# Kernel optimization log

Hardware: AMD Instinct MI355X
Metric: run time of the kernel (lower is better)

Reference implementation:

```python
import jax, jax.numpy as jnp
import numpy as np

BN_EPS = 1e-3      # Keras BatchNormalization default epsilon
LRELU_ALPHA = 0.3  # Keras LeakyReLU default alpha


def _bn(x, gamma, beta, mean, var):
    # inference-mode batch norm over the feature (last) axis
    return gamma * (x - mean) * jax.lax.rsqrt(var + BN_EPS) + beta


def _gcn(x, adj, w, b):
    # spektral GCNConv: A_hat @ (X @ W) + b   (adj assumed pre-normalized)
    xw = jnp.einsum('bnf,fc->bnc', x, w)
    return jnp.einsum('bnm,bmc->bnc', adj, xw) + b


def _lrelu(x):
    return jnp.where(x >= 0, x, LRELU_ALPHA * x)


def setup_inputs() -> dict:
    key = jax.random.key(0)
    ks = jax.random.split(key, 12)
    B, N, C = 16, 1024, 256
    x = jax.random.normal(ks[0], (B, N, C), dtype=jnp.float32)
    # roughly row-normalized dense adjacency (stands in for D^-1/2 (A+I) D^-1/2)
    adj = jax.random.uniform(ks[1], (B, N, N), dtype=jnp.float32) / N
    s = 1.0 / np.sqrt(C)
    return {
        'x': x,
        'adj': adj,
        'bn1_gamma': jnp.ones((C,), jnp.float32),
        'bn1_beta': jnp.zeros((C,), jnp.float32),
        'bn1_mean': jax.random.normal(ks[2], (C,), jnp.float32) * 0.1,
        'bn1_var': jax.random.uniform(ks[3], (C,), jnp.float32) + 0.5,
        'w1': jax.random.normal(ks[4], (C, C), jnp.float32) * s,
        'b1': jnp.zeros((C,), jnp.float32),
        'bn2_gamma': jnp.ones((C,), jnp.float32),
        'bn2_beta': jnp.zeros((C,), jnp.float32),
        'bn2_mean': jax.random.normal(ks[5], (C,), jnp.float32) * 0.1,
        'bn2_var': jax.random.uniform(ks[6], (C,), jnp.float32) + 0.5,
        'w2': jax.random.normal(ks[7], (C, C), jnp.float32) * s,
        'b2': jnp.zeros((C,), jnp.float32),
        'w_skip': jax.random.normal(ks[8], (C, C), jnp.float32) * s,
        'b_skip': jnp.zeros((C,), jnp.float32),
    }


def reference(x, adj, bn1_gamma, bn1_beta, bn1_mean, bn1_var, w1, b1,
              bn2_gamma, bn2_beta, bn2_mean, bn2_var, w2, b2, w_skip, b_skip):
    h = _bn(x, bn1_gamma, bn1_beta, bn1_mean, bn1_var)          # BN(input)
    out = _lrelu(_gcn(h, adj, w1, b1))                          # GCNConv + LeakyReLU
    out = _bn(out, bn2_gamma, bn2_beta, bn2_mean, bn2_var)      # BN
    out = _lrelu(_gcn(out, adj, w2, b2))                        # GCNConv + LeakyReLU
    skip = _gcn(h, adj, w_skip, b_skip)                         # skip GCNConv on BN(input)
    # Dropout is identity at inference
    return out + skip
```

## Files before the change

### kernel.cpp

```cpp
#include <hip/hip_runtime.h>

#define LRELU_ALPHA 0.3f
#define BN_EPS 1e-3f

using u16 = unsigned short;
using u32 = unsigned int;

typedef __attribute__((ext_vector_type(8))) short bf16x8;
typedef __attribute__((ext_vector_type(4))) float f32x4;

struct alignas(8) U16x4 { u16 x, y, z, w; };

__device__ __forceinline__ u16 f2bf(float f) {
  union { float f; u32 u; } v; v.f = f;
  u32 b = v.u;
  b += 0x7FFFu + ((b >> 16) & 1u);
  return (u16)(b >> 16);
}
__device__ __forceinline__ float bf2f(u16 h) {
  union { u32 u; float f; } v; v.u = ((u32)h) << 16;
  return v.f;
}

typedef const __attribute__((address_space(1))) void* gas_ptr;
typedef __attribute__((address_space(3))) void* las_ptr;

__device__ __forceinline__ void gload16(const void* g, void* l) {
  __builtin_amdgcn_global_load_lds((gas_ptr)g, (las_ptr)l, 16, 0, 0);
}

template <int K>
__device__ __forceinline__ void gemm_core(const u16* __restrict__ A,
                                          const u16* __restrict__ B,
                                          u16* lds,
                                          f32x4 (&acc)[4][4]) {
  const int t    = threadIdx.x;
  const int lane = t & 63;
  const int wid  = t >> 6;
  const int wm   = (wid >> 1) * 64;
  const int wn   = (wid & 1) * 64;
  const int lrow = lane & 15;
  const int lk   = (lane >> 4) * 8;

  const int r0 = t >> 3;
  const int ce = (t & 7) * 8;
  const int lo = (t >> 6) * 512;

  auto stage = [&](int buf, int kt) {
    u16* ldsA = lds + buf * 16384;
    u16* ldsB = ldsA + 8192;
    const u16* gA = A + kt * 64;
    const u16* gB = B + kt * 64;
#pragma unroll
    for (int cc = 0; cc < 4; ++cc) {
      gload16(gA + (size_t)(cc * 32 + r0) * K + ce, ldsA + cc * 2048 + lo);
      gload16(gB + (size_t)(cc * 32 + r0) * K + ce, ldsB + cc * 2048 + lo);
    }
  };

  auto compute = [&](int buf) {
    const u16* As = lds + buf * 16384;
    const u16* Bs = As + 8192;
#pragma unroll
    for (int kk = 0; kk < 2; ++kk) {
      bf16x8 a[4], b[4];
#pragma unroll
      for (int i = 0; i < 4; ++i)
        a[i] = *(const bf16x8*)(As + (wm + i * 16 + lrow) * 64 + kk * 32 + lk);
#pragma unroll
      for (int i = 0; i < 4; ++i)
        b[i] = *(const bf16x8*)(Bs + (wn + i * 16 + lrow) * 64 + kk * 32 + lk);
#pragma unroll
      for (int i = 0; i < 4; ++i)
#pragma unroll
        for (int j = 0; j < 4; ++j)
          acc[i][j] = __builtin_amdgcn_mfma_f32_16x16x32_bf16(a[i], b[j], acc[i][j], 0, 0, 0);
    }
  };

  const int KT = K / 64;
  stage(0, 0);
  asm volatile("s_waitcnt vmcnt(0)" ::: "memory");
  __syncthreads();
  int cur = 0;
#pragma unroll 1
  for (int kt = 0; kt < KT - 1; ++kt) {
    stage(cur ^ 1, kt + 1);
    compute(cur);
    asm volatile("s_waitcnt vmcnt(0)" ::: "memory");
    __syncthreads();
    cur ^= 1;
  }
  compute(cur);
}

#define ACC_INIT()                                  \
  f32x4 acc[4][4];                                  \
  _Pragma("unroll") for (int i_ = 0; i_ < 4; ++i_)  \
  _Pragma("unroll") for (int j_ = 0; j_ < 4; ++j_)  \
      acc[i_][j_] = {0.f, 0.f, 0.f, 0.f};

__global__ void k_prep_bn(const float* __restrict__ g1, const float* __restrict__ be1,
                          const float* __restrict__ m1, const float* __restrict__ v1,
                          const float* __restrict__ g2, const float* __restrict__ be2,
                          const float* __restrict__ m2, const float* __restrict__ v2,
                          float* __restrict__ s1, float* __restrict__ t1,
                          float* __restrict__ s2, float* __restrict__ t2c) {
  int c = threadIdx.x;
  float a1 = g1[c] * rsqrtf(v1[c] + BN_EPS);
  s1[c] = a1; t1[c] = be1[c] - m1[c] * a1;
  float a2 = g2[c] * rsqrtf(v2[c] + BN_EPS);
  s2[c] = a2; t2c[c] = be2[c] - m2[c] * a2;
}

__global__ void k_prep_w(const float* __restrict__ w1, const float* __restrict__ wsk,
                         const float* __restrict__ w2,
                         u16* __restrict__ wcatT, u16* __restrict__ w2T) {
  int i = blockIdx.x * 256 + threadIdx.x;
  if (i < 131072) {
    int co = i >> 8, ci = i & 255;
    const float* w = (co < 256) ? w1 : wsk;
    wcatT[i] = f2bf(w[ci * 256 + (co & 255)]);
  } else if (i < 196608) {
    int k = i - 131072;
    int co = k >> 8, ci = k & 255;
    w2T[k] = f2bf(w2[ci * 256 + co]);
  }
}

__global__ void k_convert(const float* __restrict__ adj, const float* __restrict__ x,
                          const float* __restrict__ s1, const float* __restrict__ t1,
                          u16* __restrict__ adj_bf, u16* __restrict__ h_bf) {
  const int NA = 4194304;
  const int NH = 1048576;
  int stride = gridDim.x * blockDim.x;
  for (int idx = blockIdx.x * blockDim.x + threadIdx.x; idx < NA + NH; idx += stride) {
    if (idx < NA) {
      float4 v = ((const float4*)adj)[idx];
      U16x4 o = {f2bf(v.x), f2bf(v.y), f2bf(v.z), f2bf(v.w)};
      ((U16x4*)adj_bf)[idx] = o;
    } else {
      int k = idx - NA;
      float4 v = ((const float4*)x)[k];
      int c = (k << 2) & 255;
      U16x4 o = {f2bf(v.x * s1[c] + t1[c]),     f2bf(v.y * s1[c + 1] + t1[c + 1]),
                 f2bf(v.z * s1[c + 2] + t1[c + 2]), f2bf(v.w * s1[c + 3] + t1[c + 3])};
      ((U16x4*)h_bf)[k] = o;
    }
  }
}

__global__ __launch_bounds__(256) void k_xw(const u16* __restrict__ h_bf,
                                            const u16* __restrict__ wcatT,
                                            u16* __restrict__ hwT) {
  __shared__ u16 lds[32768];
  ACC_INIT();
  const int mt = blockIdx.x, nt = blockIdx.y;
  gemm_core<256>(h_bf + (size_t)mt * 128 * 256, wcatT + (size_t)nt * 128 * 256, lds, acc);

  const int t = threadIdx.x, lane = t & 63, wid = t >> 6;
  const int rm0 = mt * 128 + (wid >> 1) * 64 + (lane >> 4) * 4;
  const int cn0 = nt * 128 + (wid & 1) * 64 + (lane & 15);
#pragma unroll
  for (int i = 0; i < 4; ++i) {
    int mm = rm0 + i * 16;
    int b = mm >> 10, n0 = mm & 1023;
#pragma unroll
    for (int j = 0; j < 4; ++j) {
      int co = cn0 + j * 16;
      U16x4 p = {f2bf(acc[i][j][0]), f2bf(acc[i][j][1]), f2bf(acc[i][j][2]), f2bf(acc[i][j][3])};
      *(U16x4*)(hwT + (((size_t)(b * 512 + co)) << 10) + n0) = p;
    }
  }
}

__global__ __launch_bounds__(256) void k_big1(const u16* __restrict__ adj_bf,
                                              const u16* __restrict__ hwT,
                                              const float* __restrict__ b1,
                                              const float* __restrict__ bsk,
                                              const float* __restrict__ s2,
                                              const float* __restrict__ t2c,
                                              u16* __restrict__ u2b,
                                              float* __restrict__ outp) {
  __shared__ u16 lds[32768];
  ACC_INIT();
  const int mt = blockIdx.x, nt = blockIdx.y, bz = blockIdx.z;
  gemm_core<1024>(adj_bf + ((size_t)bz << 20) + (size_t)mt * 128 * 1024,
                  hwT    + ((size_t)bz << 19) + (size_t)nt * 128 * 1024, lds, acc);

  const int t = threadIdx.x, lane = t & 63, wid = t >> 6;
  const int rn0 = mt * 128 + (wid >> 1) * 64 + (lane >> 4) * 4;
  const int cn0 = nt * 128 + (wid & 1) * 64 + (lane & 15);
#pragma unroll
  for (int j = 0; j < 4; ++j) {
    int c = cn0 + j * 16;
    if (c < 256) {
      float bias = b1[c], sc = s2[c], tc = t2c[c];
      u16* dst = u2b + ((size_t)bz << 18) + c;
#pragma unroll
      for (int i = 0; i < 4; ++i)
#pragma unroll
        for (int r = 0; r < 4; ++r) {
          int n = rn0 + i * 16 + r;
          float y = acc[i][j][r] + bias;
          float u = (y >= 0.f) ? y : LRELU_ALPHA * y;
          dst[(size_t)n << 8] = f2bf(u * sc + tc);
        }
    } else {
      int cc = c - 256;
      float bias = bsk[cc];
      float* dst = outp + ((size_t)bz << 18) + cc;
#pragma unroll
      for (int i = 0; i < 4; ++i)
#pragma unroll
        for (int r = 0; r < 4; ++r) {
          int n = rn0 + i * 16 + r;
          dst[(size_t)n << 8] = acc[i][j][r] + bias;
        }
    }
  }
}

__global__ __launch_bounds__(256) void k_sm2(const u16* __restrict__ w2T,
                                             const u16* __restrict__ u2b,
                                             u16* __restrict__ t2T) {
  __shared__ u16 lds[32768];
  ACC_INIT();
  const int mt = blockIdx.x, nt = blockIdx.y, bz = blockIdx.z;
  gemm_core<256>(w2T + (size_t)mt * 128 * 256,
                 u2b + ((size_t)bz << 18) + (size_t)nt * 128 * 256, lds, acc);

  const int t = threadIdx.x, lane = t & 63, wid = t >> 6;
  const int rc0 = mt * 128 + (wid >> 1) * 64 + (lane >> 4) * 4;
  const int nn0 = nt * 128 + (wid & 1) * 64 + (lane & 15);
  u16* base = t2T + ((size_t)bz << 18);
#pragma unroll
  for (int i = 0; i < 4; ++i)
#pragma unroll
    for (int j = 0; j < 4; ++j) {
      int n = nn0 + j * 16;
#pragma unroll
      for (int r = 0; r < 4; ++r) {
        int co = rc0 + i * 16 + r;
        base[((size_t)co << 10) + n] = f2bf(acc[i][j][r]);
      }
    }
}

__global__ __launch_bounds__(256) void k_big2(const u16* __restrict__ adj_bf,
                                              const u16* __restrict__ t2T,
                                              const float* __restrict__ b2,
                                              float* __restrict__ outp) {
  __shared__ u16 lds[32768];
  ACC_INIT();
  const int mt = blockIdx.x, nt = blockIdx.y, bz = blockIdx.z;
  gemm_core<1024>(adj_bf + ((size_t)bz << 20) + (size_t)mt * 128 * 1024,
                  t2T    + ((size_t)bz << 18) + (size_t)nt * 128 * 1024, lds, acc);

  const int t = threadIdx.x, lane = t & 63, wid = t >> 6;
  const int rn0 = mt * 128 + (wid >> 1) * 64 + (lane >> 4) * 4;
  const int cn0 = nt * 128 + (wid & 1) * 64 + (lane & 15);
#pragma unroll
  for (int j = 0; j < 4; ++j) {
    int c = cn0 + j * 16;
    float bias = b2[c];
#pragma unroll
    for (int i = 0; i < 4; ++i)
#pragma unroll
      for (int r = 0; r < 4; ++r) {
        int n = rn0 + i * 16 + r;
        size_t off = ((size_t)bz << 18) + ((size_t)n << 8) + c;
        float y = acc[i][j][r] + bias;
        float o = ((y >= 0.f) ? y : LRELU_ALPHA * y) + outp[off];
        outp[off] = o;
      }
  }
}

extern "C" void kernel_launch(void* const* d_in, const int* in_sizes, int n_in,
                              void* d_out, int out_size, void* d_ws, size_t ws_size,
                              hipStream_t stream) {
  const float* x   = (const float*)d_in[0];
  const float* adj = (const float*)d_in[1];
  const float* g1  = (const float*)d_in[2];
  const float* be1 = (const float*)d_in[3];
  const float* mu1 = (const float*)d_in[4];
  const float* v1  = (const float*)d_in[5];
  const float* w1  = (const float*)d_in[6];
  const float* b1  = (const float*)d_in[7];
  const float* g2  = (const float*)d_in[8];
  const float* be2 = (const float*)d_in[9];
  const float* mu2 = (const float*)d_in[10];
  const float* v2  = (const float*)d_in[11];
  const float* w2  = (const float*)d_in[12];
  const float* b2  = (const float*)d_in[13];
  const float* wsk = (const float*)d_in[14];
  const float* bsk = (const float*)d_in[15];
  float* out = (float*)d_out;

  char* ws = (char*)d_ws;
  u16*   adj_bf = (u16*)(ws);
  u16*   hwT    = (u16*)(ws + 33554432);
  u16*   h_bf   = (u16*)(ws + 50331648);
  u16*   u2b    = (u16*)(ws + 58720256);
  u16*   t2T    = (u16*)(ws + 67108864);
  u16*   wcatT  = (u16*)(ws + 75497472);
  u16*   w2T    = (u16*)(ws + 75759616);
  float* s1     = (float*)(ws + 75890688);
  float* t1     = (float*)(ws + 75891712);
  float* s2     = (float*)(ws + 75892736);
  float* t2c    = (float*)(ws + 75893760);
  if (ws_size < 75894784) return;

  k_prep_bn<<<1, 256, 0, stream>>>(g1, be1, mu1, v1, g2, be2, mu2, v2, s1, t1, s2, t2c);
  k_prep_w <<<768, 256, 0, stream>>>(w1, wsk, w2, wcatT, w2T);
  k_convert<<<2048, 256, 0, stream>>>(adj, x, s1, t1, adj_bf, h_bf);
  k_xw  <<<dim3(128, 4),    256, 0, stream>>>(h_bf, wcatT, hwT);
  k_big1<<<dim3(8, 4, 16),  256, 0, stream>>>(adj_bf, hwT, b1, bsk, s2, t2c, u2b, out);
  k_sm2 <<<dim3(2, 8, 16),  256, 0, stream>>>(w2T, u2b, t2T);
  k_big2<<<dim3(8, 2, 16),  256, 0, stream>>>(adj_bf, t2T, b2, out);
}
```

Measured before the change: 219.0 us.

## Stage GEMM epilogues through LDS for coalesced vector stores; store skip branch as bf16

Every GEMM epilogue (xw, big1, sm2, big2) now writes its accumulator tile into LDS and then issues coalesced 16-byte row stores. Before, each thread wrote scattered 2- or 4-byte values with large strides. The skip branch result is now kept as a bf16 workspace buffer rather than fp32 in the output, which halves that write and the later read in k_big2. The two prep kernels are merged into one launch. The cost is extra LDS traffic and barriers, plus reduced precision on the skip path.

```diff
diff --git a/kernel.cpp b/kernel.cpp
--- a/kernel.cpp
+++ b/kernel.cpp
@@ -100,22 +100,27 @@
   _Pragma("unroll") for (int j_ = 0; j_ < 4; ++j_)  \
       acc[i_][j_] = {0.f, 0.f, 0.f, 0.f};
 
-__global__ void k_prep_bn(const float* __restrict__ g1, const float* __restrict__ be1,
-                          const float* __restrict__ m1, const float* __restrict__ v1,
-                          const float* __restrict__ g2, const float* __restrict__ be2,
-                          const float* __restrict__ m2, const float* __restrict__ v2,
-                          float* __restrict__ s1, float* __restrict__ t1,
-                          float* __restrict__ s2, float* __restrict__ t2c) {
-  int c = threadIdx.x;
-  float a1 = g1[c] * rsqrtf(v1[c] + BN_EPS);
-  s1[c] = a1; t1[c] = be1[c] - m1[c] * a1;
-  float a2 = g2[c] * rsqrtf(v2[c] + BN_EPS);
-  s2[c] = a2; t2c[c] = be2[c] - m2[c] * a2;
-}
-
-__global__ void k_prep_w(const float* __restrict__ w1, const float* __restrict__ wsk,
-                         const float* __restrict__ w2,
-                         u16* __restrict__ wcatT, u16* __restrict__ w2T) {
+#define EPI_COORDS()                                          \
+  const int t = threadIdx.x, lane = t & 63, wid = t >> 6;     \
+  const int row0 = (wid >> 1) * 64 + (lane >> 4) * 4;         \
+  const int col0 = (wid & 1) * 64 + (lane & 15);
+
+__global__ void k_prep(const float* __restrict__ w1, const float* __restrict__ wsk,
+                       const float* __restrict__ w2,
+                       const float* __restrict__ g1, const float* __restrict__ be1,
+                       const float* __restrict__ m1, const float* __restrict__ v1,
+                       const float* __restrict__ g2, const float* __restrict__ be2,
+                       const float* __restrict__ m2, const float* __restrict__ v2,
+                       u16* __restrict__ wcatT, u16* __restrict__ w2T,
+                       float* __restrict__ s1, float* __restrict__ t1,
+                       float* __restrict__ s2, float* __restrict__ t2c) {
+  if (blockIdx.x == 0) {
+    int c = threadIdx.x;
+    float a1 = g1[c] * rsqrtf(v1[c] + BN_EPS);
+    s1[c] = a1; t1[c] = be1[c] - m1[c] * a1;
+    float a2 = g2[c] * rsqrtf(v2[c] + BN_EPS);
+    s2[c] = a2; t2c[c] = be2[c] - m2[c] * a2;
+  }
   int i = blockIdx.x * 256 + threadIdx.x;
   if (i < 131072) {
     int co = i >> 8, ci = i & 255;
@@ -143,7 +148,7 @@
       int k = idx - NA;
       float4 v = ((const float4*)x)[k];
       int c = (k << 2) & 255;
-      U16x4 o = {f2bf(v.x * s1[c] + t1[c]),     f2bf(v.y * s1[c + 1] + t1[c + 1]),
+      U16x4 o = {f2bf(v.x * s1[c] + t1[c]),         f2bf(v.y * s1[c + 1] + t1[c + 1]),
                  f2bf(v.z * s1[c + 2] + t1[c + 2]), f2bf(v.w * s1[c + 3] + t1[c + 3])};
       ((U16x4*)h_bf)[k] = o;
     }
@@ -158,19 +163,26 @@
   const int mt = blockIdx.x, nt = blockIdx.y;
   gemm_core<256>(h_bf + (size_t)mt * 128 * 256, wcatT + (size_t)nt * 128 * 256, lds, acc);
 
-  const int t = threadIdx.x, lane = t & 63, wid = t >> 6;
-  const int rm0 = mt * 128 + (wid >> 1) * 64 + (lane >> 4) * 4;
-  const int cn0 = nt * 128 + (wid & 1) * 64 + (lane & 15);
-#pragma unroll
-  for (int i = 0; i < 4; ++i) {
-    int mm = rm0 + i * 16;
-    int b = mm >> 10, n0 = mm & 1023;
-#pragma unroll
-    for (int j = 0; j < 4; ++j) {
-      int co = cn0 + j * 16;
-      U16x4 p = {f2bf(acc[i][j][0]), f2bf(acc[i][j][1]), f2bf(acc[i][j][2]), f2bf(acc[i][j][3])};
-      *(U16x4*)(hwT + (((size_t)(b * 512 + co)) << 10) + n0) = p;
-    }
+  EPI_COORDS();
+  __syncthreads();
+  u16* tl = lds;
+#pragma unroll
+  for (int j = 0; j < 4; ++j) {
+    int co_l = col0 + j * 16;
+#pragma unroll
+    for (int i = 0; i < 4; ++i)
+#pragma unroll
+      for (int r = 0; r < 4; ++r)
+        tl[co_l * 136 + row0 + i * 16 + r] = f2bf(acc[i][j][r]);
+  }
+  __syncthreads();
+  const int rw = t >> 4, seg = t & 15;
+  const int b = mt >> 3, nb = (mt & 7) * 128;
+#pragma unroll
+  for (int p = 0; p < 8; ++p) {
+    int co_l = p * 16 + rw;
+    *(bf16x8*)(hwT + (((size_t)(b * 512 + nt * 128 + co_l)) << 10) + nb + seg * 8) =
+        *(const bf16x8*)(tl + co_l * 136 + seg * 8);
   }
 }
 
@@ -181,43 +193,48 @@
                                               const float* __restrict__ s2,
                                               const float* __restrict__ t2c,
                                               u16* __restrict__ u2b,
-                                              float* __restrict__ outp) {
+                                              u16* __restrict__ skipb) {
   __shared__ u16 lds[32768];
   ACC_INIT();
   const int mt = blockIdx.x, nt = blockIdx.y, bz = blockIdx.z;
   gemm_core<1024>(adj_bf + ((size_t)bz << 20) + (size_t)mt * 128 * 1024,
                   hwT    + ((size_t)bz << 19) + (size_t)nt * 128 * 1024, lds, acc);
 
-  const int t = threadIdx.x, lane = t & 63, wid = t >> 6;
-  const int rn0 = mt * 128 + (wid >> 1) * 64 + (lane >> 4) * 4;
-  const int cn0 = nt * 128 + (wid & 1) * 64 + (lane & 15);
+  EPI_COORDS();
+  const bool conv = (nt < 2);
+  const int cb = (nt & 1) * 128;
+  __syncthreads();
+  u16* tl = lds;
 #pragma unroll
   for (int j = 0; j < 4; ++j) {
-    int c = cn0 + j * 16;
-    if (c < 256) {
-      float bias = b1[c], sc = s2[c], tc = t2c[c];
-      u16* dst = u2b + ((size_t)bz << 18) + c;
-#pragma unroll
-      for (int i = 0; i < 4; ++i)
-#pragma unroll
-        for (int r = 0; r < 4; ++r) {
-          int n = rn0 + i * 16 + r;
-          float y = acc[i][j][r] + bias;
+    int cl = col0 + j * 16;
+    int c = cb + cl;
+    float bias = conv ? b1[c] : bsk[c];
+    float sc = s2[c], tc = t2c[c];
+#pragma unroll
+    for (int i = 0; i < 4; ++i)
+#pragma unroll
+      for (int r = 0; r < 4; ++r) {
+        float y = acc[i][j][r] + bias;
+        float v;
+        if (conv) {
           float u = (y >= 0.f) ? y : LRELU_ALPHA * y;
-          dst[(size_t)n << 8] = f2bf(u * sc + tc);
+          v = fmaf(u, sc, tc);
+        } else {
+          v = y;
         }
-    } else {
-      int cc = c - 256;
-      float bias = bsk[cc];
-      float* dst = outp + ((size_t)bz << 18) + cc;
-#pragma unroll
-      for (int i = 0; i < 4; ++i)
-#pragma unroll
-        for (int r = 0; r < 4; ++r) {
-          int n = rn0 + i * 16 + r;
-          dst[(size_t)n << 8] = acc[i][j][r] + bias;
-        }
-    }
+        tl[(row0 + i * 16 + r) * 136 + cl] = f2bf(v);
+      }
+  }
+  __syncthreads();
+  u16* dstbase = (conv ? u2b : skipb) + ((size_t)bz << 18) + cb;
+  const int rw = t >> 4, seg = t & 15;
+  const int nb = mt * 128;
+#pragma unroll
+  for (int p = 0; p < 8; ++p) {
+    int nl = p * 16 + rw;
+    *(bf16x8*)(dstbase + ((size_t)(nb + nl) << 8) + seg * 8) =
+        *(const bf16x8*)(tl + nl * 136 + seg * 8);
   }
 }
 
@@ -230,26 +247,33 @@
   gemm_core<256>(w2T + (size_t)mt * 128 * 256,
                  u2b + ((size_t)bz << 18) + (size_t)nt * 128 * 256, lds, acc);
 
-  const int t = threadIdx.x, lane = t & 63, wid = t >> 6;
-  const int rc0 = mt * 128 + (wid >> 1) * 64 + (lane >> 4) * 4;
-  const int nn0 = nt * 128 + (wid & 1) * 64 + (lane & 15);
-  u16* base = t2T + ((size_t)bz << 18);
-#pragma unroll
-  for (int i = 0; i < 4; ++i)
-#pragma unroll
-    for (int j = 0; j < 4; ++j) {
-      int n = nn0 + j * 16;
-#pragma unroll
-      for (int r = 0; r < 4; ++r) {
-        int co = rc0 + i * 16 + r;
-        base[((size_t)co << 10) + n] = f2bf(acc[i][j][r]);
-      }
-    }
+  EPI_COORDS();
+  __syncthreads();
+  u16* tl = lds;
+#pragma unroll
+  for (int j = 0; j < 4; ++j) {
+    int nl = col0 + j * 16;
+#pragma unroll
+    for (int i = 0; i < 4; ++i)
+#pragma unroll
+      for (int r = 0; r < 4; ++r)
+        tl[(row0 + i * 16 + r) * 136 + nl] = f2bf(acc[i][j][r]);
+  }
+  __syncthreads();
+  const int rw = t >> 4, seg = t & 15;
+  u16* base = t2T + ((size_t)bz << 18) + nt * 128;
+#pragma unroll
+  for (int p = 0; p < 8; ++p) {
+    int co_l = p * 16 + rw;
+    *(bf16x8*)(base + (((size_t)(mt * 128 + co_l)) << 10) + seg * 8) =
+        *(const bf16x8*)(tl + co_l * 136 + seg * 8);
+  }
 }
 
 __global__ __launch_bounds__(256) void k_big2(const u16* __restrict__ adj_bf,
                                               const u16* __restrict__ t2T,
                                               const float* __restrict__ b2,
+                                              const u16* __restrict__ skipb,
                                               float* __restrict__ outp) {
   __shared__ u16 lds[32768];
   ACC_INIT();
@@ -257,23 +281,32 @@
   gemm_core<1024>(adj_bf + ((size_t)bz << 20) + (size_t)mt * 128 * 1024,
                   t2T    + ((size_t)bz << 18) + (size_t)nt * 128 * 1024, lds, acc);
 
-  const int t = threadIdx.x, lane = t & 63, wid = t >> 6;
-  const int rn0 = mt * 128 + (wid >> 1) * 64 + (lane >> 4) * 4;
-  const int cn0 = nt * 128 + (wid & 1) * 64 + (lane & 15);
+  EPI_COORDS();
+  __syncthreads();
+  float* tf = (float*)lds;
 #pragma unroll
   for (int j = 0; j < 4; ++j) {
-    int c = cn0 + j * 16;
-    float bias = b2[c];
+    int cl = col0 + j * 16;
+    float bias = b2[nt * 128 + cl];
 #pragma unroll
     for (int i = 0; i < 4; ++i)
 #pragma unroll
       for (int r = 0; r < 4; ++r) {
-        int n = rn0 + i * 16 + r;
-        size_t off = ((size_t)bz << 18) + ((size_t)n << 8) + c;
         float y = acc[i][j][r] + bias;
-        float o = ((y >= 0.f) ? y : LRELU_ALPHA * y) + outp[off];
-        outp[off] = o;
+        tf[(row0 + i * 16 + r) * 128 + cl] = (y >= 0.f) ? y : LRELU_ALPHA * y;
       }
+  }
+  __syncthreads();
+  const int rw = t >> 5, seg = t & 31;
+  const int cbase = nt * 128;
+#pragma unroll
+  for (int p = 0; p < 16; ++p) {
+    int nl = p * 8 + rw;
+    size_t go = ((size_t)bz << 18) + ((size_t)(mt * 128 + nl) << 8) + cbase + seg * 4;
+    float4 v = *(const float4*)(tf + nl * 128 + seg * 4);
+    U16x4 sk = *(const U16x4*)(skipb + go);
+    float4 o = {v.x + bf2f(sk.x), v.y + bf2f(sk.y), v.z + bf2f(sk.z), v.w + bf2f(sk.w)};
+    *(float4*)(outp + go) = o;
   }
 }
 
@@ -304,19 +337,20 @@
   u16*   h_bf   = (u16*)(ws + 50331648);
   u16*   u2b    = (u16*)(ws + 58720256);
   u16*   t2T    = (u16*)(ws + 67108864);
-  u16*   wcatT  = (u16*)(ws + 75497472);
-  u16*   w2T    = (u16*)(ws + 75759616);
-  float* s1     = (float*)(ws + 75890688);
-  float* t1     = (float*)(ws + 75891712);
-  float* s2     = (float*)(ws + 75892736);
-  float* t2c    = (float*)(ws + 75893760);
-  if (ws_size < 75894784) return;
-
-  k_prep_bn<<<1, 256, 0, stream>>>(g1, be1, mu1, v1, g2, be2, mu2, v2, s1, t1, s2, t2c);
-  k_prep_w <<<768, 256, 0, stream>>>(w1, wsk, w2, wcatT, w2T);
+  u16*   skipb  = (u16*)(ws + 75497472);
+  u16*   wcatT  = (u16*)(ws + 83886080);
+  u16*   w2T    = (u16*)(ws + 84148224);
+  float* s1     = (float*)(ws + 84279296);
+  float* t1     = (float*)(ws + 84280320);
+  float* s2     = (float*)(ws + 84281344);
+  float* t2c    = (float*)(ws + 84282368);
+  if (ws_size < 84283392) return;
+
+  k_prep   <<<768, 256, 0, stream>>>(w1, wsk, w2, g1, be1, mu1, v1, g2, be2, mu2, v2,
+                                     wcatT, w2T, s1, t1, s2, t2c);
   k_convert<<<2048, 256, 0, stream>>>(adj, x, s1, t1, adj_bf, h_bf);
-  k_xw  <<<dim3(128, 4),    256, 0, stream>>>(h_bf, wcatT, hwT);
-  k_big1<<<dim3(8, 4, 16),  256, 0, stream>>>(adj_bf, hwT, b1, bsk, s2, t2c, u2b, out);
-  k_sm2 <<<dim3(2, 8, 16),  256, 0, stream>>>(w2T, u2b, t2T);
-  k_big2<<<dim3(8, 2, 16),  256, 0, stream>>>(adj_bf, t2T, b2, out);
-}
+  k_xw  <<<dim3(128, 4),   256, 0, stream>>>(h_bf, wcatT, hwT);
+  k_big1<<<dim3(8, 4, 16), 256, 0, stream>>>(adj_bf, hwT, b1, bsk, s2, t2c, u2b, skipb);
+  k_sm2 <<<dim3(2, 8, 16), 256, 0, stream>>>(w2T, u2b, t2T);
+  k_big2<<<dim3(8, 2, 16), 256, 0, stream>>>(adj_bf, t2T, b2, skipb, out);
+}
```

Measured after the change: 216.9 us. No clear change (-1.0%).
